# Kernel optimization log

Hardware: AMD Instinct MI355X
Metric: run time of the kernel (lower is better)

## Reference

```python
import jax, jax.numpy as jnp
import numpy as np

NUM_HEADS = 12
OT_REG = 0.1
SINKHORN_ITERS = 10
DIAG_VAL = 1e3


def setup_inputs() -> dict:
    key = jax.random.key(0)
    k1, k2, k3 = jax.random.split(key, 3)
    B, N, C = 64, 256, 768
    x = jax.random.normal(k1, (B, N, C), dtype=jnp.float32)
    w_qkv = jax.random.normal(k2, (3 * C, C), dtype=jnp.float32) * (C ** -0.5)
    w_proj = jax.random.normal(k3, (C, C), dtype=jnp.float32) * (C ** -0.5)
    b_proj = jnp.zeros((C,), dtype=jnp.float32)
    return {"x": x, "w_qkv": w_qkv, "w_proj": w_proj, "b_proj": b_proj}


def _sot(q):
    # q: [B, H, N, hd] -> self-optimal-transport plan [B, H, N, N]
    N = q.shape[-2]
    qn = q / (jnp.linalg.norm(q, axis=-1, keepdims=True) + 1e-8)
    C = 1.0 - jnp.einsum('bhnd,bhmd->bhnm', qn, qn)          # cosine cost
    eye = jnp.eye(N, dtype=bool)
    C = jnp.where(eye, DIAG_VAL, C)                            # mask diagonal
    log_K = -C / OT_REG
    log_marg = -jnp.log(jnp.float32(N))                        # uniform r = c = 1/N
    log_v = jnp.zeros(q.shape[:2] + (N,), dtype=q.dtype)
    for _ in range(SINKHORN_ITERS):
        log_u = log_marg - jax.nn.logsumexp(log_K + log_v[..., None, :], axis=-1)
        log_v = log_marg - jax.nn.logsumexp(log_K + log_u[..., :, None], axis=-2)
    log_T = log_u[..., :, None] + log_K + log_v[..., None, :]
    z = jnp.exp(log_T)
    z = z / jnp.max(z, axis=(-2, -1), keepdims=True)           # max_scale per sample/head
    z = jnp.where(eye, 1.0, z)                                 # diagonal set to 1
    return z


def reference(x, w_qkv, w_proj, b_proj):
    B, N, C = x.shape
    H = NUM_HEADS
    hd = C // H
    scale = hd ** -0.5
    qkv = jnp.einsum('bnc,oc->bno', x, w_qkv)                  # [B, N, 3C]
    qkv = qkv.reshape(B, N, 3, H, hd).transpose(2, 0, 3, 1, 4)  # [3, B, H, N, hd]
    q, k, v = qkv[0], qkv[1], qkv[2]
    attn = _sot(q)                                              # [B, H, N, N]
    attn = jax.nn.softmax(attn * scale, axis=-1)               # dropout = identity (eval)
    out = jnp.einsum('bhnm,bhmd->bhnd', attn, v)
    out = out.transpose(0, 2, 1, 3).reshape(B, N, C)
    out = jnp.einsum('bnc,oc->bno', out, w_proj) + b_proj
    return out
```

## Files before the change

### kernel.cpp

```cpp
#include <hip/hip_runtime.h>

typedef unsigned short u16;
typedef unsigned int   u32;
typedef __attribute__((ext_vector_type(8))) short bf16x8;
typedef __attribute__((ext_vector_type(4))) float f32x4;

__device__ __forceinline__ u16 f2bf(float f) {
    u32 u = __float_as_uint(f);
    u += 0x7fffu + ((u >> 16) & 1u);
    return (u16)(u >> 16);
}
__device__ __forceinline__ float bf2f(u16 s) {
    return __uint_as_float(((u32)s) << 16);
}
__device__ __forceinline__ u32 pack2bf(float f0, float f1) {
    return (u32)f2bf(f0) | ((u32)f2bf(f1) << 16);
}
__device__ __forceinline__ u32 cvtpk2bf(float f0, float f1) {
    u32 r;
    asm("v_cvt_pk_bf16_f32 %0, %1, %2" : "=v"(r) : "v"(f0), "v"(f1));
    return r;
}

__device__ __forceinline__ void gload_lds16(const void* g, void* l) {
    __builtin_amdgcn_global_load_lds(
        (const __attribute__((address_space(1))) u32*)g,
        (__attribute__((address_space(3))) u32*)l, 16, 0, 0);
}

__global__ __launch_bounds__(256)
void conv_bf16(const float* __restrict__ src, u16* __restrict__ dst, int n8)
{
    const int i = blockIdx.x * 256 + threadIdx.x;
    if (i < n8) {
        const float4 a = ((const float4*)src)[2*i];
        const float4 b = ((const float4*)src)[2*i + 1];
        ((uint4*)dst)[i] = make_uint4(pack2bf(a.x,a.y), pack2bf(a.z,a.w),
                                      pack2bf(b.x,b.y), pack2bf(b.z,b.w));
    }
}

__global__ __launch_bounds__(256)
void conv_wqv(const float* __restrict__ w, u16* __restrict__ dst)
{
    const int i = blockIdx.x * 256 + threadIdx.x;
    const int row = i / 96;
    const int cc  = (i - row * 96) * 8;
    const int srow = row + (row >= 768 ? 768 : 0);
    const float4 a = *(const float4*)&w[(size_t)srow*768 + cc];
    const float4 b = *(const float4*)&w[(size_t)srow*768 + cc + 4];
    *(uint4*)&dst[(size_t)row*768 + cc] =
        make_uint4(pack2bf(a.x,a.y), pack2bf(a.z,a.w), pack2bf(b.x,b.y), pack2bf(b.z,b.w));
}

__device__ __forceinline__ void mfma_gemm_core(
    const char* __restrict__ Arow0,
    const char* __restrict__ Brow0,
    u16* As, u16* Bs, const int tid, f32x4 acc[4][4])
{
    const int l  = tid & 63, w = tid >> 6;
    const int wr = w >> 1,  wc = w & 1;
    char* Asb = (char*)As;
    char* Bsb = (char*)Bs;
    const int co = 16 * ((l & 7) ^ (l >> 3));
    const size_t rstep = (size_t)(l >> 3) * 1536;
    const int rsw = (l & 7) << 4;

    for (int k0 = 0; k0 < 1536; k0 += 128) {
        #pragma unroll
        for (int i = 0; i < 4; ++i) {
            const int rb = i*32 + w*8;
            gload_lds16(Arow0 + (size_t)rb*1536 + rstep + k0 + co, Asb + i*4096 + w*1024);
            gload_lds16(Brow0 + (size_t)rb*1536 + rstep + k0 + co, Bsb + i*4096 + w*1024);
        }
        __syncthreads();
        bf16x8 af[2][4], bfr[2][4];
        #pragma unroll
        for (int kk = 0; kk < 2; ++kk) {
            const int coff = (kk*64 + ((l >> 4) << 4)) ^ rsw;
            #pragma unroll
            for (int mi = 0; mi < 4; ++mi) {
                const int rowA = wr*64 + mi*16 + (l & 15);
                af[kk][mi]  = *(const bf16x8*)(Asb + rowA*128 + coff);
                const int rowB = wc*64 + mi*16 + (l & 15);
                bfr[kk][mi] = *(const bf16x8*)(Bsb + rowB*128 + coff);
            }
        }
        #pragma unroll
        for (int mi = 0; mi < 4; ++mi)
            #pragma unroll
            for (int nj = 0; nj < 4; ++nj) {
                acc[mi][nj] = __builtin_amdgcn_mfma_f32_16x16x32_bf16(
                                  af[0][mi], bfr[0][nj], acc[mi][nj], 0, 0, 0);
                acc[mi][nj] = __builtin_amdgcn_mfma_f32_16x16x32_bf16(
                                  af[1][mi], bfr[1][nj], acc[mi][nj], 0, 0, 0);
            }
        __syncthreads();
    }
}

__global__ __launch_bounds__(256)
void gemm_qkv_mfma(const u16* __restrict__ xbf, const u16* __restrict__ wqv,
                   u16* __restrict__ qnbf, u16* __restrict__ vbfT)
{
    __shared__ u16 As[128*64];
    __shared__ u16 Bs[128*64];
    const int m0 = blockIdx.x * 128;
    const int bj = blockIdx.y;
    const int tid = threadIdx.x;
    f32x4 acc[4][4];
    #pragma unroll
    for (int i = 0; i < 4; ++i)
        #pragma unroll
        for (int j = 0; j < 4; ++j) acc[i][j] = (f32x4){0.f,0.f,0.f,0.f};

    mfma_gemm_core((const char*)xbf + (size_t)m0*1536,
                   (const char*)wqv + (size_t)bj*128*1536,
                   As, Bs, tid, acc);

    const int l = tid & 63, w = tid >> 6;
    const int wr = w >> 1, wc = w & 1;
    const int rbase = m0 + wr*64 + ((l >> 4) << 2);
    if (bj < 6) {
        const int h = 2*bj + wc;
        #pragma unroll
        for (int mi = 0; mi < 4; ++mi)
            #pragma unroll
            for (int rr = 0; rr < 4; ++rr) {
                float s =      acc[mi][0][rr]*acc[mi][0][rr];
                s = fmaf(acc[mi][1][rr], acc[mi][1][rr], s);
                s = fmaf(acc[mi][2][rr], acc[mi][2][rr], s);
                s = fmaf(acc[mi][3][rr], acc[mi][3][rr], s);
                #pragma unroll
                for (int off = 1; off < 16; off <<= 1) s += __shfl_xor(s, off);
                const float inv = 1.0f / (sqrtf(s) + 1e-8f);
                const int m = rbase + mi*16 + rr;
                const int b_ = m >> 8, n_ = m & 255;
                u16* row = qnbf + ((((size_t)b_*12 + h) << 8) + n_)*64;
                #pragma unroll
                for (int nj = 0; nj < 4; ++nj)
                    row[nj*16 + (l & 15)] = f2bf(acc[mi][nj][rr] * inv);
            }
    } else {
        const int colb = (bj - 6)*128 + wc*64;
        #pragma unroll
        for (int mi = 0; mi < 4; ++mi)
            #pragma unroll
            for (int nj = 0; nj < 4; ++nj) {
                const int col = colb + nj*16 + (l & 15);
                const int h = col >> 6, d = col & 63;
                const int m = rbase + mi*16;
                const int b_ = m >> 8, n_ = m & 255;
                uint2 o = make_uint2(pack2bf(acc[mi][nj][0], acc[mi][nj][1]),
                                     pack2bf(acc[mi][nj][2], acc[mi][nj][3]));
                *(uint2*)&vbfT[(((size_t)b_*12 + h)*64 + d)*256 + n_] = o;
            }
    }
}

__global__ __launch_bounds__(256)
void gemm_proj_mfma(const u16* __restrict__ ctxb, const u16* __restrict__ wpb,
                    const float* __restrict__ bias, float* __restrict__ out)
{
    __shared__ u16 As[128*64];
    __shared__ u16 Bs[128*64];
    const int m0 = blockIdx.x * 128;
    const int n0 = blockIdx.y * 128;
    const int tid = threadIdx.x;
    f32x4 acc[4][4];
    #pragma unroll
    for (int i = 0; i < 4; ++i)
        #pragma unroll
        for (int j = 0; j < 4; ++j) acc[i][j] = (f32x4){0.f,0.f,0.f,0.f};

    mfma_gemm_core((const char*)ctxb + (size_t)m0*1536,
                   (const char*)wpb + (size_t)n0*1536,
                   As, Bs, tid, acc);

    const int l = tid & 63, w = tid >> 6;
    const int wr = w >> 1, wc = w & 1;
    const int rbase = m0 + wr*64 + ((l >> 4) << 2);
    #pragma unroll
    for (int mi = 0; mi < 4; ++mi)
        #pragma unroll
        for (int nj = 0; nj < 4; ++nj) {
            const int col = n0 + wc*64 + nj*16 + (l & 15);
            const float bv = bias[col];
            #pragma unroll
            for (int rr = 0; rr < 4; ++rr) {
                const int m = rbase + mi*16 + rr;
                out[(size_t)m*768 + col] = acc[mi][nj][rr] + bv;
            }
        }
}

__global__ __launch_bounds__(256)
void cost_kernel(const u16* __restrict__ qnbf, u16* __restrict__ Kmat)
{
    __shared__ u16 Qa[128*64];
    __shared__ u16 Qb[128*64];
    const int bh = blockIdx.y;
    const int tr = (blockIdx.x >> 1) * 128;
    const int tc = (blockIdx.x & 1) * 128;
    const char* qb = (const char*)(qnbf + (size_t)bh * 16384);
    const int tid = threadIdx.x;
    const int l = tid & 63, w = tid >> 6;
    const int wr = w >> 1, wc = w & 1;

    {
        const int co = ((l & 7) ^ (l >> 3)) << 4;
        const int rl = l >> 3;
        #pragma unroll
        for (int i = 0; i < 4; ++i) {
            const int ch = i*4 + w;
            gload_lds16(qb + (size_t)(tr + ch*8 + rl)*128 + co, (char*)Qa + ch*1024);
            gload_lds16(qb + (size_t)(tc + ch*8 + rl)*128 + co, (char*)Qb + ch*1024);
        }
    }
    __syncthreads();

    f32x4 acc[4][4];
    #pragma unroll
    for (int i = 0; i < 4; ++i)
        #pragma unroll
        for (int j = 0; j < 4; ++j) acc[i][j] = (f32x4){0.f,0.f,0.f,0.f};

    bf16x8 af[2][4], bfr[2][4];
    #pragma unroll
    for (int kk = 0; kk < 2; ++kk) {
        const int kb = kk*64 + ((l >> 4) << 4);
        #pragma unroll
        for (int f = 0; f < 4; ++f) {
            const int ra = wr*64 + f*16 + (l & 15);
            af[kk][f]  = *(const bf16x8*)((char*)Qa + ra*128 + (kb ^ ((ra & 7) << 4)));
            const int rb = wc*64 + f*16 + (l & 15);
            bfr[kk][f] = *(const bf16x8*)((char*)Qb + rb*128 + (kb ^ ((rb & 7) << 4)));
        }
    }
    #pragma unroll
    for (int mi = 0; mi < 4; ++mi)
        #pragma unroll
        for (int nj = 0; nj < 4; ++nj) {
            acc[mi][nj] = __builtin_amdgcn_mfma_f32_16x16x32_bf16(
                              af[0][mi], bfr[0][nj], acc[mi][nj], 0, 0, 0);
            acc[mi][nj] = __builtin_amdgcn_mfma_f32_16x16x32_bf16(
                              af[1][mi], bfr[1][nj], acc[mi][nj], 0, 0, 0);
        }

    u16* Kb = Kmat + (size_t)bh * 65536;
    #pragma unroll
    for (int mi = 0; mi < 4; ++mi)
        #pragma unroll
        for (int nj = 0; nj < 4; ++nj) {
            const int gr0 = tr + wr*64 + mi*16 + ((l >> 4) << 2);
            const int gc  = tc + wc*64 + nj*16 + (l & 15);
            #pragma unroll
            for (int rr = 0; rr < 4; ++rr) {
                const int gr = gr0 + rr;
                const float s = acc[mi][nj][rr];
                const float km = (gr == gc) ? 0.f : __expf(fmaf(10.f, s, -10.f));
                Kb[(size_t)gr * 256 + gc] = f2bf(km);
            }
        }
}

__global__ __launch_bounds__(512, 2)
void sinkhorn_attn_kernel(const u16* __restrict__ Kmat, const u16* __restrict__ vbfT,
                          u16* __restrict__ ctxc)
{
    __shared__ u16 Vt[64*256];
    __shared__ __align__(16) float xv[256];
    __shared__ __align__(16) float usave[256];
    __shared__ __align__(16) u16   xbf[256];
    __shared__ float pmax[8];
    const int bh  = blockIdx.x;
    const int b_ = bh / 12, h_ = bh - b_*12;
    const int tid = threadIdx.x;
    const int l = tid & 63, w = tid >> 6;
    const int rowb = w * 32;
    const char* Kg = (const char*)(Kmat + (size_t)bh * 65536);

    {
        const char* src = (const char*)(vbfT + (size_t)bh * 16384);
        char* dst = (char*)Vt;
        const int s = l & 31;
        #pragma unroll
        for (int i = 0; i < 4; ++i) {
            const int d = i*16 + w*2 + (l >> 5);
            gload_lds16(src + d*512 + ((s ^ (d & 7)) << 4), dst + i*8192 + w*1024);
        }
    }

    bf16x8 kf[2][8];
    {
        const char* kb0 = Kg + (size_t)(rowb + (l & 15)) * 512 + ((l >> 4) << 4);
        #pragma unroll
        for (int t = 0; t < 2; ++t)
            #pragma unroll
            for (int ks = 0; ks < 8; ++ks)
                kf[t][ks] = *(const bf16x8*)(kb0 + t*8192 + ks*64);
    }
    if (tid < 256) xbf[tid] = 0x3f80;
    __syncthreads();

    for (int it = 0; it < 20; ++it) {
        f32x4 a0a = {0.f,0.f,0.f,0.f}, a0b = {0.f,0.f,0.f,0.f};
        f32x4 a1a = {0.f,0.f,0.f,0.f}, a1b = {0.f,0.f,0.f,0.f};
        #pragma unroll
        for (int ks = 0; ks < 4; ++ks) {
            const bf16x8 xf = *(const bf16x8*)((const char*)xbf + ks*64 + ((l >> 4) << 4));
            a0a = __builtin_amdgcn_mfma_f32_16x16x32_bf16(kf[0][ks], xf, a0a, 0, 0, 0);
            a1a = __builtin_amdgcn_mfma_f32_16x16x32_bf16(kf[1][ks], xf, a1a, 0, 0, 0);
        }
        #pragma unroll
        for (int ks = 4; ks < 8; ++ks) {
            const bf16x8 xf = *(const bf16x8*)((const char*)xbf + ks*64 + ((l >> 4) << 4));
            a0b = __builtin_amdgcn_mfma_f32_16x16x32_bf16(kf[0][ks], xf, a0b, 0, 0, 0);
            a1b = __builtin_amdgcn_mfma_f32_16x16x32_bf16(kf[1][ks], xf, a1b, 0, 0, 0);
        }
        float xn0[4], xn1[4];
        #pragma unroll
        for (int j = 0; j < 4; ++j) {
            xn0[j] = 0.00390625f * __builtin_amdgcn_rcpf(a0a[j] + a0b[j]);
            xn1[j] = 0.00390625f * __builtin_amdgcn_rcpf(a1a[j] + a1b[j]);
        }
        const u32 xp0 = cvtpk2bf(xn0[0], xn0[1]);
        const u32 xp1 = cvtpk2bf(xn0[2], xn0[3]);
        const u32 xp2 = cvtpk2bf(xn1[0], xn1[1]);
        const u32 xp3 = cvtpk2bf(xn1[2], xn1[3]);
        if ((l & 15) == 0) {
            const int r0 = rowb + ((l >> 4) << 2);
            *(uint2*)&xbf[r0]      = make_uint2(xp0, xp1);
            *(uint2*)&xbf[r0 + 16] = make_uint2(xp2, xp3);
            if (it == 18) {
                *(float4*)&usave[r0]      = make_float4(xn0[0], xn0[1], xn0[2], xn0[3]);
                *(float4*)&usave[r0 + 16] = make_float4(xn1[0], xn1[1], xn1[2], xn1[3]);
            }
            if (it == 19) {
                *(float4*)&xv[r0]      = make_float4(xn0[0], xn0[1], xn0[2], xn0[3]);
                *(float4*)&xv[r0 + 16] = make_float4(xn1[0], xn1[1], xn1[2], xn1[3]);
            }
        }
        __syncthreads();
    }

    {
        float mx0 = 0.f, mx1 = 0.f;
        #pragma unroll
        for (int ks = 0; ks < 8; ++ks) {
            const int mbase = ks*32 + ((l >> 4) << 3);
            const float4 va  = *(const float4*)&xv[mbase];
            const float4 vb4 = *(const float4*)&xv[mbase + 4];
            const float vv[8] = {va.x, va.y, va.z, va.w, vb4.x, vb4.y, vb4.z, vb4.w};
            #pragma unroll
            for (int j = 0; j < 8; ++j) {
                mx0 = fmaxf(mx0, bf2f((u16)kf[0][ks][j]) * vv[j]);
                mx1 = fmaxf(mx1, bf2f((u16)kf[1][ks][j]) * vv[j]);
            }
        }
        float mx = fmaxf(usave[rowb + (l & 15)] * mx0,
                         usave[rowb + 16 + (l & 15)] * mx1);
        #pragma unroll
        for (int off = 32; off > 0; off >>= 1) mx = fmaxf(mx, __shfl_xor(mx, off));
        if (l == 0) pmax[w] = mx;
    }
    __syncthreads();
    float tm = pmax[0];
    #pragma unroll
    for (int i = 1; i < 8; ++i) tm = fmaxf(tm, pmax[i]);
    const float itmax = 1.0f / tm;

    u16* outp = ctxc + ((size_t)b_*256)*768 + h_*64;
    #pragma unroll
    for (int t = 0; t < 2; ++t) {
        const int rown = rowb + t*16 + (l & 15);
        const float an = usave[rown] * itmax * 0.125f;
        float psum = 0.f;
        f32x4 acc0 = {0.f,0.f,0.f,0.f}, acc1 = {0.f,0.f,0.f,0.f};
        f32x4 acc2 = {0.f,0.f,0.f,0.f}, acc3 = {0.f,0.f,0.f,0.f};
        #pragma unroll
        for (int ks = 0; ks < 8; ++ks) {
            const int mbase = ks*32 + ((l >> 4) << 3);
            const float4 va  = *(const float4*)&xv[mbase];
            const float4 vb4 = *(const float4*)&xv[mbase + 4];
            const float vv[8] = {va.x, va.y, va.z, va.w, vb4.x, vb4.y, vb4.z, vb4.w};
            float p[8];
            #pragma unroll
            for (int j = 0; j < 8; ++j)
                p[j] = __expf(an * bf2f((u16)kf[t][ks][j]) * vv[j]);
            const int dj = rown - mbase;
            if (dj >= 0 && dj < 8) p[dj] = 1.13314845f;
            psum += ((p[0]+p[1]) + (p[2]+p[3])) + ((p[4]+p[5]) + (p[6]+p[7]));
            uint4 pwv = make_uint4(cvtpk2bf(p[0], p[1]), cvtpk2bf(p[2], p[3]),
                                   cvtpk2bf(p[4], p[5]), cvtpk2bf(p[6], p[7]));
            const bf16x8 pf = *(const bf16x8*)&pwv;
            const int bc = ks*64 + ((l >> 4) << 4);
            {
                const int d = (l & 15);
                const bf16x8 vf = *(const bf16x8*)((char*)Vt + d*512 + (bc ^ ((d & 7) << 4)));
                acc0 = __builtin_amdgcn_mfma_f32_16x16x32_bf16(vf, pf, acc0, 0, 0, 0);
            }
            {
                const int d = 16 + (l & 15);
                const bf16x8 vf = *(const bf16x8*)((char*)Vt + d*512 + (bc ^ ((d & 7) << 4)));
                acc1 = __builtin_amdgcn_mfma_f32_16x16x32_bf16(vf, pf, acc1, 0, 0, 0);
            }
            {
                const int d = 32 + (l & 15);
                const bf16x8 vf = *(const bf16x8*)((char*)Vt + d*512 + (bc ^ ((d & 7) << 4)));
                acc2 = __builtin_amdgcn_mfma_f32_16x16x32_bf16(vf, pf, acc2, 0, 0, 0);
            }
            {
                const int d = 48 + (l & 15);
                const bf16x8 vf = *(const bf16x8*)((char*)Vt + d*512 + (bc ^ ((d & 7) << 4)));
                acc3 = __builtin_amdgcn_mfma_f32_16x16x32_bf16(vf, pf, acc3, 0, 0, 0);
            }
        }
        psum += __shfl_xor(psum, 16);
        psum += __shfl_xor(psum, 32);
        const float is = 1.0f / psum;
        const int d0 = (l >> 4) << 2;
        uint2 o0 = make_uint2(cvtpk2bf(acc0[0]*is, acc0[1]*is), cvtpk2bf(acc0[2]*is, acc0[3]*is));
        uint2 o1 = make_uint2(cvtpk2bf(acc1[0]*is, acc1[1]*is), cvtpk2bf(acc1[2]*is, acc1[3]*is));
        uint2 o2 = make_uint2(cvtpk2bf(acc2[0]*is, acc2[1]*is), cvtpk2bf(acc2[2]*is, acc2[3]*is));
        uint2 o3 = make_uint2(cvtpk2bf(acc3[0]*is, acc3[1]*is), cvtpk2bf(acc3[2]*is, acc3[3]*is));
        u16* orow = outp + (size_t)rown*768;
        *(uint2*)&orow[d0]      = o0;
        *(uint2*)&orow[16 + d0] = o1;
        *(uint2*)&orow[32 + d0] = o2;
        *(uint2*)&orow[48 + d0] = o3;
    }
}

extern "C" void kernel_launch(void* const* d_in, const int* in_sizes, int n_in,
                              void* d_out, int out_size, void* d_ws, size_t ws_size,
                              hipStream_t stream)
{
    (void)in_sizes; (void)n_in; (void)out_size; (void)ws_size;
    const float* x      = (const float*)d_in[0];
    const float* w_qkv  = (const float*)d_in[1];
    const float* w_proj = (const float*)d_in[2];
    const float* b_proj = (const float*)d_in[3];
    float* out = (float*)d_out;

    char* w = (char*)d_ws;
    u16*   xbf  = (u16*)  (w);
    u16*   wqv  = (u16*)  (w + 25165824);
    u16*   wpb  = (u16*)  (w + 27525120);
    u16*   qnbf = (u16*)  (w + 28704768);
    u16*   vbfT = (u16*)  (w + 79036416);
    u16*   ctxc = (u16*)  (w + 104202240);
    u16*   Km   = (u16*)  (w + 130944000);

    conv_bf16           <<<dim3(6144),    256, 0, stream>>>(x, xbf, 1572864);
    conv_wqv            <<<dim3(576),     256, 0, stream>>>(w_qkv, wqv);
    conv_bf16           <<<dim3(288),     256, 0, stream>>>(w_proj, wpb, 73728);
    gemm_qkv_mfma       <<<dim3(128, 12), 256, 0, stream>>>(xbf, wqv, qnbf, vbfT);
    cost_kernel         <<<dim3(4, 768),  256, 0, stream>>>(qnbf, Km);
    sinkhorn_attn_kernel<<<dim3(768),     512, 0, stream>>>(Km, vbfT, ctxc);
    gemm_proj_mfma      <<<dim3(128, 6),  256, 0, stream>>>(ctxc, wpb, b_proj, out);
}
```

Measured before the change: 222.4 us.

## Split fused Sinkhorn-attention kernel into separate Sinkhorn and PV kernels

Splits the fused kernel in two. One kernel runs the Sinkhorn iterations and writes the u, v scaling vectors and the per-head max to workspace. A second kernel reloads K and V and computes the softmax-weighted PV product. This removes the 32KB V tile from the Sinkhorn kernel's shared memory, which may allow higher occupancy during the iteration loop. The cost is reading the K matrix from global memory a second time, plus an extra launch.

```diff
diff --git a/kernel.cpp b/kernel.cpp
--- a/kernel.cpp
+++ b/kernel.cpp
@@ -265,31 +265,18 @@
 }
 
 __global__ __launch_bounds__(512, 2)
-void sinkhorn_attn_kernel(const u16* __restrict__ Kmat, const u16* __restrict__ vbfT,
-                          u16* __restrict__ ctxc)
-{
-    __shared__ u16 Vt[64*256];
+void sinkhorn_kernel(const u16* __restrict__ Kmat, float* __restrict__ ubuf,
+                     float* __restrict__ vbuf, float* __restrict__ tmaxbuf)
+{
     __shared__ __align__(16) float xv[256];
     __shared__ __align__(16) float usave[256];
     __shared__ __align__(16) u16   xbf[256];
     __shared__ float pmax[8];
     const int bh  = blockIdx.x;
-    const int b_ = bh / 12, h_ = bh - b_*12;
     const int tid = threadIdx.x;
     const int l = tid & 63, w = tid >> 6;
     const int rowb = w * 32;
     const char* Kg = (const char*)(Kmat + (size_t)bh * 65536);
-
-    {
-        const char* src = (const char*)(vbfT + (size_t)bh * 16384);
-        char* dst = (char*)Vt;
-        const int s = l & 31;
-        #pragma unroll
-        for (int i = 0; i < 4; ++i) {
-            const int d = i*16 + w*2 + (l >> 5);
-            gload_lds16(src + d*512 + ((s ^ (d & 7)) << 4), dst + i*8192 + w*1024);
-        }
-    }
 
     bf16x8 kf[2][8];
     {
@@ -365,16 +352,63 @@
         if (l == 0) pmax[w] = mx;
     }
     __syncthreads();
-    float tm = pmax[0];
-    #pragma unroll
-    for (int i = 1; i < 8; ++i) tm = fmaxf(tm, pmax[i]);
-    const float itmax = 1.0f / tm;
+    if (tid < 256) {
+        ubuf[bh * 256 + tid] = usave[tid];
+        vbuf[bh * 256 + tid] = xv[tid];
+    }
+    if (tid == 0) {
+        float tm = pmax[0];
+        #pragma unroll
+        for (int i = 1; i < 8; ++i) tm = fmaxf(tm, pmax[i]);
+        tmaxbuf[bh] = tm;
+    }
+}
+
+__global__ __launch_bounds__(512, 2)
+void pv_kernel(const u16* __restrict__ Kmat, const u16* __restrict__ vbfT,
+               const float* __restrict__ ubuf, const float* __restrict__ vbuf,
+               const float* __restrict__ tmaxbuf, u16* __restrict__ ctxc)
+{
+    __shared__ u16 Vt[64*256];
+    __shared__ __align__(16) float xv[256];
+    const int bh  = blockIdx.x;
+    const int b_ = bh / 12, h_ = bh - b_*12;
+    const int tid = threadIdx.x;
+    const int l = tid & 63, w = tid >> 6;
+    const int rowb = w * 32;
+    const char* Kg = (const char*)(Kmat + (size_t)bh * 65536);
+
+    {
+        const char* src = (const char*)(vbfT + (size_t)bh * 16384);
+        char* dst = (char*)Vt;
+        const int s = l & 31;
+        #pragma unroll
+        for (int i = 0; i < 4; ++i) {
+            const int d = i*16 + w*2 + (l >> 5);
+            gload_lds16(src + d*512 + ((s ^ (d & 7)) << 4), dst + i*8192 + w*1024);
+        }
+    }
+    if (tid < 256) xv[tid] = vbuf[bh*256 + tid];
+
+    bf16x8 kf[2][8];
+    {
+        const char* kb0 = Kg + (size_t)(rowb + (l & 15)) * 512 + ((l >> 4) << 4);
+        #pragma unroll
+        for (int t = 0; t < 2; ++t)
+            #pragma unroll
+            for (int ks = 0; ks < 8; ++ks)
+                kf[t][ks] = *(const bf16x8*)(kb0 + t*8192 + ks*64);
+    }
+    const float itmax = 1.0f / tmaxbuf[bh];
+    const float u0 = ubuf[bh*256 + rowb + (l & 15)];
+    const float u1 = ubuf[bh*256 + rowb + 16 + (l & 15)];
+    __syncthreads();
 
     u16* outp = ctxc + ((size_t)b_*256)*768 + h_*64;
     #pragma unroll
     for (int t = 0; t < 2; ++t) {
         const int rown = rowb + t*16 + (l & 15);
-        const float an = usave[rown] * itmax * 0.125f;
+        const float an = (t == 0 ? u0 : u1) * itmax * 0.125f;
         float psum = 0.f;
         f32x4 acc0 = {0.f,0.f,0.f,0.f}, acc1 = {0.f,0.f,0.f,0.f};
         f32x4 acc2 = {0.f,0.f,0.f,0.f}, acc3 = {0.f,0.f,0.f,0.f};
@@ -450,13 +484,17 @@
     u16*   qnbf = (u16*)  (w + 28704768);
     u16*   vbfT = (u16*)  (w + 79036416);
     u16*   ctxc = (u16*)  (w + 104202240);
+    float* ub   = (float*)(w + 129368064);
+    float* vb   = (float*)(w + 130154496);
+    float* tmx  = (float*)(w + 130940928);
     u16*   Km   = (u16*)  (w + 130944000);
 
-    conv_bf16           <<<dim3(6144),    256, 0, stream>>>(x, xbf, 1572864);
-    conv_wqv            <<<dim3(576),     256, 0, stream>>>(w_qkv, wqv);
-    conv_bf16           <<<dim3(288),     256, 0, stream>>>(w_proj, wpb, 73728);
-    gemm_qkv_mfma       <<<dim3(128, 12), 256, 0, stream>>>(xbf, wqv, qnbf, vbfT);
-    cost_kernel         <<<dim3(4, 768),  256, 0, stream>>>(qnbf, Km);
-    sinkhorn_attn_kernel<<<dim3(768),     512, 0, stream>>>(Km, vbfT, ctxc);
-    gemm_proj_mfma      <<<dim3(128, 6),  256, 0, stream>>>(ctxc, wpb, b_proj, out);
-}
+    conv_bf16      <<<dim3(6144),    256, 0, stream>>>(x, xbf, 1572864);
+    conv_wqv       <<<dim3(576),     256, 0, stream>>>(w_qkv, wqv);
+    conv_bf16      <<<dim3(288),     256, 0, stream>>>(w_proj, wpb, 73728);
+    gemm_qkv_mfma  <<<dim3(128, 12), 256, 0, stream>>>(xbf, wqv, qnbf, vbfT);
+    cost_kernel    <<<dim3(4, 768),  256, 0, stream>>>(qnbf, Km);
+    sinkhorn_kernel<<<dim3(768),     512, 0, stream>>>(Km, ub, vb, tmx);
+    pv_kernel      <<<dim3(768),     512, 0, stream>>>(Km, vbfT, ub, vb, tmx, ctxc);
+    gemm_proj_mfma <<<dim3(128, 6),  256, 0, stream>>>(ctxc, wpb, b_proj, out);
+}
```

New measurement: 219.6 us. About the same (-1.3%).
